# Kernel tuning notes

Measured on AMD Instinct MI355X. Metric: run time of the kernel, lower is better.

## Reference

```python
import jax, jax.numpy as jnp
import numpy as np

ALPHA = 0.2      # LeakyReLU negative slope
NEG_INF = -9e15  # mask value from the original module
EPS = 1e-8


def setup_inputs() -> dict:
    key = jax.random.key(0)
    k1, k2, k3, k4 = jax.random.split(key, 4)
    B, N, F_in, F_out = 8, 2048, 128, 64
    h = jax.random.normal(k1, (B, N, F_in), dtype=jnp.float32)
    u = jax.random.uniform(k2, (B, N, N), dtype=jnp.float32)
    adj = jnp.where(u > 0.9, u, 0.0)
    adj = jnp.maximum(adj, jnp.eye(N, dtype=jnp.float32)[None])
    # Xavier-uniform with gain 1.414 as in the torch init
    gain = 1.414
    bW = gain * np.sqrt(6.0 / (F_in + F_out))
    W = jax.random.uniform(k3, (F_in, F_out), jnp.float32, -bW, bW)
    ba = gain * np.sqrt(6.0 / (2 * F_out + 1))
    a = jax.random.uniform(k4, (2 * F_out, 1), jnp.float32, -ba, ba)
    return {"h": h, "adj": adj, "W": W, "a": a}


def reference(h, adj, W, a):
    # h: [B,N,Fin], adj: [B,N,N], W: [Fin,Fout], a: [2*Fout,1]
    F_out = W.shape[1]
    Wh = jnp.einsum('bnf,fo->bno', h, W)                      # [B,N,Fout]
    # Split-projection equivalent of cat([Wh_i, Wh_j]) @ a:
    # e[b,i,j] = leaky(Wh[b,i]@a1 + Wh[b,j]@a2)
    a1 = a[:F_out, 0]
    a2 = a[F_out:, 0]
    e = jax.nn.leaky_relu(
        (Wh @ a1)[:, :, None] + (Wh @ a2)[:, None, :],        # [B,N,N]
        negative_slope=ALPHA,
    )
    att = jnp.where(adj > 0, e, NEG_INF)
    att = jax.nn.softmax(att, axis=2)
    att = att * adj
    att = att / (jnp.sum(att, axis=2, keepdims=True) + EPS)
    h_prime = jnp.einsum('bij,bjo->bio', att, Wh)             # [B,N,Fout]
    return jax.nn.elu(h_prime)                                # concat=True -> ELU
```

## Files before the change

kernel.cpp:

```cpp
#include <hip/hip_runtime.h>
#include <hip/hip_bf16.h>
#include <stdint.h>

#define LRELU_ALPHA 0.2f
#define L2E 1.44269504f

constexpr int BB = 8, NN = 2048, FIN = 128, FOUT = 64;
constexpr int GEMM_ROWS = 32;
constexpr int NBLK_G = BB * NN / GEMM_ROWS;

typedef __attribute__((ext_vector_type(8))) short short8;
typedef __attribute__((ext_vector_type(4))) float f32x4;

__device__ __forceinline__ ushort bf16rn(float f) {
    __hip_bfloat16 h = __float2bfloat16(f);
    return *reinterpret_cast<ushort*>(&h);
}

#define HS 132
__global__ __launch_bounds__(256) void k_gemm_hw(const float* __restrict__ h,
                                                 const float* __restrict__ W,
                                                 const float* __restrict__ a,
                                                 ushort* __restrict__ WhP,
                                                 float* __restrict__ s1,
                                                 float* __restrict__ s2,
                                                 float* __restrict__ pmax) {
    __shared__ float hs[GEMM_ROWS * HS];
    __shared__ float smax[16];
    const int tid = threadIdx.x;
    const int base = blockIdx.x * GEMM_ROWS;

    #pragma unroll
    for (int rep = 0; rep < 4; ++rep) {
        int flat4 = rep * 256 + tid;
        int row = flat4 >> 5, k4 = flat4 & 31;
        float4 v = *reinterpret_cast<const float4*>(h + (size_t)(base + row) * FIN + k4 * 4);
        *reinterpret_cast<float4*>(&hs[row * HS + k4 * 4]) = v;
    }
    __syncthreads();

    const int tr = tid >> 4;
    const int tc = tid & 15;
    float acc[2][4] = {};
    #pragma unroll 4
    for (int k = 0; k < FIN; ++k) {
        float4 wv = *reinterpret_cast<const float4*>(W + (size_t)k * FOUT + tc * 4);
        #pragma unroll
        for (int r = 0; r < 2; ++r) {
            float hv = hs[(tr * 2 + r) * HS + k];
            acc[r][0] = fmaf(hv, wv.x, acc[r][0]);
            acc[r][1] = fmaf(hv, wv.y, acc[r][1]);
            acc[r][2] = fmaf(hv, wv.z, acc[r][2]);
            acc[r][3] = fmaf(hv, wv.w, acc[r][3]);
        }
    }

    const int b = base >> 11;
    const int jbase = base & 2047;
    #pragma unroll
    for (int r = 0; r < 2; ++r) {
        const int jloc = jbase + tr * 2 + r;
        const int e = jloc & 7;
        const int kgrp = (jloc >> 3) & 3;
        const int jblk = jloc >> 5;
        #pragma unroll
        for (int c = 0; c < 4; ++c) {
            const int col = tc * 4 + c;
            size_t off = ((((size_t)b * 64 + jblk) * 4 + (col >> 4)) * 64 + kgrp * 16 + (col & 15)) * 8 + e;
            WhP[off] = bf16rn(acc[r][c]);
        }
    }

    float a1c[4], a2c[4];
    #pragma unroll
    for (int c = 0; c < 4; ++c) {
        a1c[c] = a[tc * 4 + c];
        a2c[c] = a[FOUT + tc * 4 + c];
    }
    float maxp2 = -3.4e38f;
    #pragma unroll
    for (int r = 0; r < 2; ++r) {
        float p1 = acc[r][0] * a1c[0] + acc[r][1] * a1c[1] + acc[r][2] * a1c[2] + acc[r][3] * a1c[3];
        float p2 = acc[r][0] * a2c[0] + acc[r][1] * a2c[1] + acc[r][2] * a2c[2] + acc[r][3] * a2c[3];
        #pragma unroll
        for (int off = 1; off < 16; off <<= 1) {
            p1 += __shfl_xor(p1, off);
            p2 += __shfl_xor(p2, off);
        }
        if (tc == 0) {
            s1[base + tr * 2 + r] = p1;
            s2[base + tr * 2 + r] = p2;
            maxp2 = fmaxf(maxp2, p2);
        }
    }
    if (tc == 0) smax[tr] = maxp2;
    __syncthreads();
    if (tid == 0) {
        float m = smax[0];
        #pragma unroll
        for (int i = 1; i < 16; ++i) m = fmaxf(m, smax[i]);
        pmax[blockIdx.x] = m;
    }
}

__global__ __launch_bounds__(256, 4) void k_attn(const float* __restrict__ adj,
                                                 const ushort* __restrict__ WhP,
                                                 const float* __restrict__ s1,
                                                 const float* __restrict__ s2,
                                                 const float* __restrict__ pmax,
                                                 float* __restrict__ out) {
    __shared__ float lacc[4][16][68];
    __shared__ float lS[4][16];

    const int tid = threadIdx.x;
    const int l = tid & 63, w = tid >> 6;
    const int li = l & 15, lk = l >> 4;
    const int blk = blockIdx.x;
    const int b = blk >> 7;
    const int rowbase = blk * 16;
    const int row_i = rowbase + li;

    float m = -3.4e38f;
    #pragma unroll
    for (int t = 0; t < 8; ++t) m = fmaxf(m, pmax[l + 64 * t]);
    #pragma unroll
    for (int off = 32; off > 0; off >>= 1) m = fmaxf(m, __shfl_xor(m, off));

    const float s1i = s1[row_i];
    const float cp = s1i + m;
    const float c = fmaxf(cp, LRELU_ALPHA * cp);
    const float cL = c * L2E;

    const float* __restrict__ adjp = adj + (size_t)row_i * NN + w * 512 + lk * 8;
    const float* __restrict__ s2p  = s2 + (size_t)b * NN + w * 512 + lk * 8;
    const ushort* __restrict__ whp = WhP + (size_t)b * 131072 + (size_t)(w * 16) * 2048 + l * 8;

    f32x4 acc0 = {0.f, 0.f, 0.f, 0.f};
    f32x4 acc1 = {0.f, 0.f, 0.f, 0.f};
    f32x4 acc2 = {0.f, 0.f, 0.f, 0.f};
    f32x4 acc3 = {0.f, 0.f, 0.f, 0.f};
    float Sp = 0.f;

    float4 pa[2][2];
    pa[0][0] = *reinterpret_cast<const float4*>(adjp);
    pa[0][1] = *reinterpret_cast<const float4*>(adjp + 4);
    pa[1][0] = *reinterpret_cast<const float4*>(adjp + 32);
    pa[1][1] = *reinterpret_cast<const float4*>(adjp + 36);

    #pragma unroll
    for (int t = 0; t < 16; ++t) {
        const float4 a0 = pa[t & 1][0];
        const float4 a1 = pa[t & 1][1];
        if (t + 2 < 16) {
            pa[t & 1][0] = *reinterpret_cast<const float4*>(adjp + (t + 2) * 32);
            pa[t & 1][1] = *reinterpret_cast<const float4*>(adjp + (t + 2) * 32 + 4);
        }
        const float4 v0 = *reinterpret_cast<const float4*>(s2p + t * 32);
        const float4 v1 = *reinterpret_cast<const float4*>(s2p + t * 32 + 4);
        const ushort* p_ = whp + t * 2048;
        const short8 b0 = *reinterpret_cast<const short8*>(p_);
        const short8 b1 = *reinterpret_cast<const short8*>(p_ + 512);
        const short8 b2 = *reinterpret_cast<const short8*>(p_ + 1024);
        const short8 b3 = *reinterpret_cast<const short8*>(p_ + 1536);

        const float aa[8] = {a0.x, a0.y, a0.z, a0.w, a1.x, a1.y, a1.z, a1.w};
        const float ss[8] = {v0.x, v0.y, v0.z, v0.w, v1.x, v1.y, v1.z, v1.w};
        short8 af;
        #pragma unroll
        for (int e = 0; e < 8; ++e) {
            float ev = s1i + ss[e];
            float lr = fmaxf(ev, LRELU_ALPHA * ev);
            float ex = exp2f(fmaf(lr, L2E, -cL));
            float wv = aa[e] * ex;
            ushort ub = bf16rn(wv);
            Sp += __uint_as_float((uint32_t)ub << 16);
            af[e] = (short)ub;
        }
        acc0 = __builtin_amdgcn_mfma_f32_16x16x32_bf16(af, b0, acc0, 0, 0, 0);
        acc1 = __builtin_amdgcn_mfma_f32_16x16x32_bf16(af, b1, acc1, 0, 0, 0);
        acc2 = __builtin_amdgcn_mfma_f32_16x16x32_bf16(af, b2, acc2, 0, 0, 0);
        acc3 = __builtin_amdgcn_mfma_f32_16x16x32_bf16(af, b3, acc3, 0, 0, 0);
    }

    float Sred = Sp;
    Sred += __shfl_xor(Sred, 16);
    Sred += __shfl_xor(Sred, 32);
    if (l < 16) lS[w][li] = Sred;

    const f32x4 accs[4] = {acc0, acc1, acc2, acc3};
    #pragma unroll
    for (int r = 0; r < 4; ++r)
        #pragma unroll
        for (int tt = 0; tt < 4; ++tt)
            lacc[w][lk * 4 + r][tt * 16 + li] = accs[tt][r];

    __syncthreads();

    #pragma unroll
    for (int q = 0; q < 4; ++q) {
        const int idx = q * 256 + tid;
        const int row = idx >> 6, col = idx & 63;
        float v = lacc[0][row][col] + lacc[1][row][col] + lacc[2][row][col] + lacc[3][row][col];
        float S = lS[0][row] + lS[1][row] + lS[2][row] + lS[3][row];
        float o = v / S;
        o = o > 0.f ? o : expm1f(o);
        out[(size_t)(rowbase + row) * FOUT + col] = o;
    }
}

extern "C" void kernel_launch(void* const* d_in, const int* in_sizes, int n_in,
                              void* d_out, int out_size, void* d_ws, size_t ws_size,
                              hipStream_t stream) {
    (void)in_sizes; (void)n_in; (void)out_size; (void)ws_size;
    const float* h   = (const float*)d_in[0];
    const float* adj = (const float*)d_in[1];
    const float* W   = (const float*)d_in[2];
    const float* a   = (const float*)d_in[3];
    float* out = (float*)d_out;

    ushort* WhP = (ushort*)d_ws;
    float* s1w  = (float*)(WhP + (size_t)BB * NN * FOUT);
    float* s2w  = s1w + (size_t)BB * NN;
    float* pmaxw = s2w + (size_t)BB * NN;

    k_gemm_hw<<<NBLK_G, 256, 0, stream>>>(h, W, a, WhP, s1w, s2w, pmaxw);
    k_attn<<<BB * NN / 16, 256, 0, stream>>>(adj, WhP, s1w, s2w, pmaxw, out);
}
```

Baseline: 52.19 us.

## Stage Wh fragments in LDS for coalesced stores; compute row sums via MFMA

The projection kernel now writes its bf16 Wh fragments into a shared-memory buffer and stores them with one 16-byte write per thread, replacing scattered 2-byte global stores. The attention kernel replaces the per-element scalar row-sum accumulation and shuffle reduction with an extra MFMA against a ones vector. It also prefetches the Wh B-fragments one step ahead alongside adjacency, changing the adjacency prefetch depth from two steps to one. This costs extra LDS and register use, and one more MFMA per iteration.

New measurement: 54.62 us. 1.05x slower.

```diff
diff --git a/kernel.cpp b/kernel.cpp
--- a/kernel.cpp
+++ b/kernel.cpp
@@ -26,6 +26,7 @@
                                                  float* __restrict__ s2,
                                                  float* __restrict__ pmax) {
     __shared__ float hs[GEMM_ROWS * HS];
+    __shared__ __align__(16) ushort fragbuf[2048];
     __shared__ float smax[16];
     const int tid = threadIdx.x;
     const int base = blockIdx.x * GEMM_ROWS;
@@ -55,19 +56,14 @@
         }
     }
 
-    const int b = base >> 11;
-    const int jbase = base & 2047;
     #pragma unroll
     for (int r = 0; r < 2; ++r) {
-        const int jloc = jbase + tr * 2 + r;
-        const int e = jloc & 7;
-        const int kgrp = (jloc >> 3) & 3;
-        const int jblk = jloc >> 5;
+        const int jloc = tr * 2 + r;
+        const int e = jloc & 7, kgrp = jloc >> 3;
         #pragma unroll
         for (int c = 0; c < 4; ++c) {
             const int col = tc * 4 + c;
-            size_t off = ((((size_t)b * 64 + jblk) * 4 + (col >> 4)) * 64 + kgrp * 16 + (col & 15)) * 8 + e;
-            WhP[off] = bf16rn(acc[r][c]);
+            fragbuf[((col >> 4) * 64 + kgrp * 16 + (col & 15)) * 8 + e] = bf16rn(acc[r][c]);
         }
     }
 
@@ -95,11 +91,16 @@
     }
     if (tc == 0) smax[tr] = maxp2;
     __syncthreads();
+
+    const size_t region = ((size_t)((base >> 11) * 64 + ((base & 2047) >> 5))) * 2048;
+    *reinterpret_cast<uint4*>(WhP + region + tid * 8) =
+        *reinterpret_cast<const uint4*>(fragbuf + tid * 8);
+
     if (tid == 0) {
-        float m = smax[0];
-        #pragma unroll
-        for (int i = 1; i < 16; ++i) m = fmaxf(m, smax[i]);
-        pmax[blockIdx.x] = m;
+        float mm = smax[0];
+        #pragma unroll
+        for (int i = 1; i < 16; ++i) mm = fmaxf(mm, smax[i]);
+        pmax[blockIdx.x] = mm;
     }
 }
 
@@ -139,60 +140,70 @@
     f32x4 acc1 = {0.f, 0.f, 0.f, 0.f};
     f32x4 acc2 = {0.f, 0.f, 0.f, 0.f};
     f32x4 acc3 = {0.f, 0.f, 0.f, 0.f};
-    float Sp = 0.f;
-
-    float4 pa[2][2];
-    pa[0][0] = *reinterpret_cast<const float4*>(adjp);
-    pa[0][1] = *reinterpret_cast<const float4*>(adjp + 4);
-    pa[1][0] = *reinterpret_cast<const float4*>(adjp + 32);
-    pa[1][1] = *reinterpret_cast<const float4*>(adjp + 36);
+    f32x4 accS = {0.f, 0.f, 0.f, 0.f};
+    short8 ones;
+    #pragma unroll
+    for (int e = 0; e < 8; ++e) ones[e] = (short)0x3F80;
+
+    float4 a0 = *reinterpret_cast<const float4*>(adjp);
+    float4 a1 = *reinterpret_cast<const float4*>(adjp + 4);
+    short8 b0 = *reinterpret_cast<const short8*>(whp);
+    short8 b1 = *reinterpret_cast<const short8*>(whp + 512);
+    short8 b2 = *reinterpret_cast<const short8*>(whp + 1024);
+    short8 b3 = *reinterpret_cast<const short8*>(whp + 1536);
 
     #pragma unroll
     for (int t = 0; t < 16; ++t) {
-        const float4 a0 = pa[t & 1][0];
-        const float4 a1 = pa[t & 1][1];
-        if (t + 2 < 16) {
-            pa[t & 1][0] = *reinterpret_cast<const float4*>(adjp + (t + 2) * 32);
-            pa[t & 1][1] = *reinterpret_cast<const float4*>(adjp + (t + 2) * 32 + 4);
+        float4 na0, na1;
+        short8 nb0, nb1, nb2, nb3;
+        if (t < 15) {
+            na0 = *reinterpret_cast<const float4*>(adjp + (t + 1) * 32);
+            na1 = *reinterpret_cast<const float4*>(adjp + (t + 1) * 32 + 4);
+            const ushort* np = whp + (t + 1) * 2048;
+            nb0 = *reinterpret_cast<const short8*>(np);
+            nb1 = *reinterpret_cast<const short8*>(np + 512);
+            nb2 = *reinterpret_cast<const short8*>(np + 1024);
+            nb3 = *reinterpret_cast<const short8*>(np + 1536);
         }
         const float4 v0 = *reinterpret_cast<const float4*>(s2p + t * 32);
         const float4 v1 = *reinterpret_cast<const float4*>(s2p + t * 32 + 4);
-        const ushort* p_ = whp + t * 2048;
-        const short8 b0 = *reinterpret_cast<const short8*>(p_);
-        const short8 b1 = *reinterpret_cast<const short8*>(p_ + 512);
-        const short8 b2 = *reinterpret_cast<const short8*>(p_ + 1024);
-        const short8 b3 = *reinterpret_cast<const short8*>(p_ + 1536);
-
-        const float aa[8] = {a0.x, a0.y, a0.z, a0.w, a1.x, a1.y, a1.z, a1.w};
-        const float ss[8] = {v0.x, v0.y, v0.z, v0.w, v1.x, v1.y, v1.z, v1.w};
+
         short8 af;
-        #pragma unroll
-        for (int e = 0; e < 8; ++e) {
-            float ev = s1i + ss[e];
-            float lr = fmaxf(ev, LRELU_ALPHA * ev);
-            float ex = exp2f(fmaf(lr, L2E, -cL));
-            float wv = aa[e] * ex;
-            ushort ub = bf16rn(wv);
-            Sp += __uint_as_float((uint32_t)ub << 16);
-            af[e] = (short)ub;
+        {
+            float ev, lr, ex;
+#define DOE(idx, AV, SV)                                                      \
+            ev = s1i + (SV);                                                  \
+            lr = fmaxf(ev, LRELU_ALPHA * ev);                                 \
+            ex = exp2f(fmaf(lr, L2E, -cL));                                   \
+            af[idx] = (short)bf16rn((AV) * ex);
+            DOE(0, a0.x, v0.x) DOE(1, a0.y, v0.y) DOE(2, a0.z, v0.z) DOE(3, a0.w, v0.w)
+            DOE(4, a1.x, v1.x) DOE(5, a1.y, v1.y) DOE(6, a1.z, v1.z) DOE(7, a1.w, v1.w)
+#undef DOE
         }
         acc0 = __builtin_amdgcn_mfma_f32_16x16x32_bf16(af, b0, acc0, 0, 0, 0);
         acc1 = __builtin_amdgcn_mfma_f32_16x16x32_bf16(af, b1, acc1, 0, 0, 0);
         acc2 = __builtin_amdgcn_mfma_f32_16x16x32_bf16(af, b2, acc2, 0, 0, 0);
         acc3 = __builtin_amdgcn_mfma_f32_16x16x32_bf16(af, b3, acc3, 0, 0, 0);
-    }
-
-    float Sred = Sp;
-    Sred += __shfl_xor(Sred, 16);
-    Sred += __shfl_xor(Sred, 32);
-    if (l < 16) lS[w][li] = Sred;
-
-    const f32x4 accs[4] = {acc0, acc1, acc2, acc3};
-    #pragma unroll
-    for (int r = 0; r < 4; ++r)
-        #pragma unroll
-        for (int tt = 0; tt < 4; ++tt)
-            lacc[w][lk * 4 + r][tt * 16 + li] = accs[tt][r];
+        accS = __builtin_amdgcn_mfma_f32_16x16x32_bf16(af, ones, accS, 0, 0, 0);
+
+        if (t < 15) {
+            a0 = na0; a1 = na1;
+            b0 = nb0; b1 = nb1; b2 = nb2; b3 = nb3;
+        }
+    }
+
+    if (li == 0) {
+        #pragma unroll
+        for (int r = 0; r < 4; ++r) lS[w][lk * 4 + r] = accS[r];
+    }
+
+    #pragma unroll
+    for (int r = 0; r < 4; ++r) {
+        lacc[w][lk * 4 + r][0 * 16 + li] = acc0[r];
+        lacc[w][lk * 4 + r][1 * 16 + li] = acc1[r];
+        lacc[w][lk * 4 + r][2 * 16 + li] = acc2[r];
+        lacc[w][lk * 4 + r][3 * 16 + li] = acc3[r];
+    }
 
     __syncthreads();
 
```
